# Performance work log

Measured on AMD Instinct MI355X. Metric: run time of the kernel, lower is better.

## Reference

```python
import jax, jax.numpy as jnp
import numpy as np

B, T, DIM = 2, 4096, 2048
H, HKV = 16, 4
HD = DIM // H          # 128
NREP = H // HKV        # 4
R = 16                 # csa_compress_ratio
TOPK = 64              # min(csa_top_k, max_seq_len // R)
THETA = 10000.0


def setup_inputs() -> dict:
    key = jax.random.key(0)
    ks = jax.random.split(key, 9)
    s = 0.02
    return {
        "x":   jax.random.normal(ks[0], (B, T, DIM), jnp.float32),
        "wq":  jax.random.normal(ks[1], (DIM, H * HD),  jnp.float32) * s,
        "wk":  jax.random.normal(ks[2], (DIM, HKV * HD), jnp.float32) * s,
        "wv":  jax.random.normal(ks[3], (DIM, HKV * HD), jnp.float32) * s,
        "wo":  jax.random.normal(ks[4], (DIM, DIM), jnp.float32) * s,
        "wiq": jax.random.normal(ks[5], (DIM, HD), jnp.float32) * s,
        "wik": jax.random.normal(ks[6], (DIM, HD), jnp.float32) * s,
        "cwa": jax.random.normal(ks[7], (HD,), jnp.float32) * s,
        "cwb": jax.random.normal(ks[8], (HD,), jnp.float32) * s,
    }


def _rope(x, cos, sin):
    # x: [B, h, T, HD]; pairs (x[2i], x[2i+1]) rotated by angle[t, i]
    half = HD // 2
    xr = x.reshape(*x.shape[:-1], half, 2)
    a, b = xr[..., 0], xr[..., 1]          # [B, h, T, half]
    ra = a * cos - b * sin                 # cos/sin: [T, half] broadcast
    rb = a * sin + b * cos
    return jnp.stack([ra, rb], axis=-1).reshape(x.shape)


def reference(x, wq, wk, wv, wo, wiq, wik, cwa, cwb):
    Bx, Tx, C = x.shape
    half = HD // 2
    # RoPE tables (buffer in original, deterministic -> recomputed here)
    freqs = 1.0 / (THETA ** (jnp.arange(half, dtype=jnp.float32) / half))
    ang = jnp.arange(Tx, dtype=jnp.float32)[:, None] * freqs[None, :]  # [T, half]
    cos, sin = jnp.cos(ang), jnp.sin(ang)

    q = (x @ wq).reshape(Bx, Tx, H, HD).transpose(0, 2, 1, 3)    # [B,H,T,HD]
    k = (x @ wk).reshape(Bx, Tx, HKV, HD).transpose(0, 2, 1, 3)  # [B,HKV,T,HD]
    v = (x @ wv).reshape(Bx, Tx, HKV, HD).transpose(0, 2, 1, 3)
    q = _rope(q, cos, sin)
    k = _rope(k, cos, sin)

    # chunked softmax-weighted KV compression (vectorized over blocks)
    nb = Tx // R
    kb = k.reshape(Bx, HKV, nb, R, HD)
    vb = v.reshape(Bx, HKV, nb, R, HD)
    wa = jax.nn.softmax(kb @ cwa, axis=-1)   # [B,HKV,nb,R], softmax within block
    wb_ = jax.nn.softmax(kb @ cwb, axis=-1)
    w = 0.5 * (wa + wb_)
    ck = jnp.einsum('bhnr,bhnrd->bhnd', w, kb)  # [B,HKV,nb,HD]
    cv = jnp.einsum('bhnr,bhnrd->bhnd', w, vb)

    # indexer: scores[b,t] = mean_j( qi[b,t] . ki[b,j] ) = qi[b,t] . mean_j ki[b,j]
    qi = x @ wiq                         # [B,T,HD]
    ki_mean = (x @ wik).mean(axis=1)     # [B,HD]
    scores = jnp.einsum('btd,bd->bt', qi, ki_mean)  # [B,T]
    block_scores = scores[:, :nb]                   # [B,nb]

    if nb > TOPK:
        idx = jax.lax.top_k(block_scores, TOPK)[1]             # [B,TOPK]
        ck = jnp.take_along_axis(ck, idx[:, None, :, None], axis=2)  # [B,HKV,TOPK,HD]
        cv = jnp.take_along_axis(cv, idx[:, None, :, None], axis=2)

    # GQA repeat + sparse attention over selected compressed blocks (no mask)
    k_rep = jnp.repeat(ck, NREP, axis=1)   # [B,H,TOPK,HD]
    v_rep = jnp.repeat(cv, NREP, axis=1)
    att = jax.nn.softmax(
        jnp.einsum('bhtd,bhsd->bhts', q, k_rep) / jnp.sqrt(jnp.float32(HD)),
        axis=-1)                            # [B,H,T,TOPK]
    out = jnp.einsum('bhts,bhsd->bhtd', att, v_rep)
    out = out.transpose(0, 2, 1, 3).reshape(Bx, Tx, C)
    return out @ wo
```

## Files before the change

kernel.cpp:

```cpp
#include <hip/hip_runtime.h>
#include <math.h>
#include <stdint.h>

#define BB    2
#define TT    4096
#define CDIM  2048
#define NHQ   16
#define NKV   4
#define HD    128
#define HALF  64
#define NREP  4
#define RBLK  16
#define NB    256
#define TOPK  64

#define MROWS (BB * TT)
#define NQKV  (CDIM + 2 * NKV * HD)
#define XELE  ((size_t)MROWS * CDIM)

typedef __bf16 bf16;
typedef __bf16 bf16x4 __attribute__((ext_vector_type(4)));
typedef __bf16 bf16x8 __attribute__((ext_vector_type(8)));
typedef float f32x4 __attribute__((ext_vector_type(4)));

typedef __attribute__((address_space(1))) unsigned int gu32;
typedef __attribute__((address_space(3))) unsigned int lu32;

__device__ __forceinline__ void gload_lds16(const void* g, void* l) {
  void* gv = const_cast<void*>(g);
  __builtin_amdgcn_global_load_lds((gu32*)gv, (lu32*)l, 16, 0, 0);
}

#define MFMA_BF16 __builtin_amdgcn_mfma_f32_16x16x32_bf16


#define LB192   28672
#define A192_AL 8192
#define A192_BH 16384
#define A192_BL 22528

__device__ __forceinline__ void mfma3_core192(const bf16* __restrict__ Ah,
                                              const bf16* __restrict__ Al,
                                              const bf16* __restrict__ Bh,
                                              const bf16* __restrict__ Bl,
                                              int bm, int bn,
                                              f32x4 acc[8][3]) {
  __shared__ __align__(16) bf16 smem[2 * LB192];
  const int tid = threadIdx.x;
  const int wave = tid >> 6, lane = tid & 63;
  const int lr4 = lane >> 2;
  const int cgs = (lane & 3) ^ ((lane >> 3) & 3);
  const size_t stageoff = (size_t)lr4 * CDIM + cgs * 8;

  const bf16* gp[7];
  int loff[7];
#pragma unroll
  for (int u = 0; u < 7; ++u) {
    int c = wave * 7 + u;
    const bf16* base;
    int lb;
    if (c < 16)      { base = Ah + (size_t)(bm + c * 16) * CDIM;        lb = c * 512; }
    else if (c < 32) { base = Al + (size_t)(bm + (c - 16) * 16) * CDIM; lb = A192_AL + (c - 16) * 512; }
    else if (c < 44) { base = Bh + (size_t)(bn + (c - 32) * 16) * CDIM; lb = A192_BH + (c - 32) * 512; }
    else             { base = Bl + (size_t)(bn + (c - 44) * 16) * CDIM; lb = A192_BL + (c - 44) * 512; }
    gp[u] = base + stageoff;
    loff[u] = lb;
  }

  const int wr = wave >> 2, wc = wave & 3;
  const int fr = lane & 15, lg = lane >> 4;
  const int chunk = (lg ^ ((fr >> 1) & 3)) << 3;
  const int arow = wr * 128 + fr;
  const int brow = wc * 48 + fr;

#pragma unroll
  for (int u = 0; u < 7; ++u) gload_lds16(gp[u], &smem[loff[u]]);

  for (int t = 0; t < 64; ++t) {
    const bf16* cb = &smem[(t & 1) * LB192];
    bf16* nb = &smem[((t + 1) & 1) * LB192];
    const int kk = (t + 1) * 32;
    const bool nlast = (t < 63);

    if (nlast) {
      gload_lds16(gp[0] + kk, nb + loff[0]);
      gload_lds16(gp[1] + kk, nb + loff[1]);
      gload_lds16(gp[2] + kk, nb + loff[2]);
      asm volatile("s_waitcnt vmcnt(3)" ::: "memory");
    } else {
      asm volatile("s_waitcnt vmcnt(0)" ::: "memory");
    }
    __builtin_amdgcn_s_barrier();
    asm volatile("" ::: "memory");

    bf16x8 fah[8], fal[8];
#pragma unroll
    for (int i = 0; i < 8; ++i) {
      fah[i] = *(const bf16x8*)&cb[(arow + i * 16) * 32 + chunk];
      fal[i] = *(const bf16x8*)&cb[A192_AL + (arow + i * 16) * 32 + chunk];
    }
    {
      bf16x8 fbh = *(const bf16x8*)&cb[A192_BH + brow * 32 + chunk];
      bf16x8 fbl = *(const bf16x8*)&cb[A192_BL + brow * 32 + chunk];
      __builtin_amdgcn_s_setprio(1);
#pragma unroll
      for (int i = 0; i < 8; ++i) {
        acc[i][0] = MFMA_BF16(fah[i], fbh, acc[i][0], 0, 0, 0);
        acc[i][0] = MFMA_BF16(fah[i], fbl, acc[i][0], 0, 0, 0);
        acc[i][0] = MFMA_BF16(fal[i], fbh, acc[i][0], 0, 0, 0);
      }
      __builtin_amdgcn_s_setprio(0);
    }
    asm volatile("" ::: "memory");
    __builtin_amdgcn_s_barrier();
    asm volatile("" ::: "memory");

#pragma unroll
    for (int j = 1; j < 3; ++j) {
      if (nlast) {
        gload_lds16(gp[2 * j + 1] + kk, nb + loff[2 * j + 1]);
        gload_lds16(gp[2 * j + 2] + kk, nb + loff[2 * j + 2]);
      }
      bf16x8 fbh = *(const bf16x8*)&cb[A192_BH + (brow + j * 16) * 32 + chunk];
      bf16x8 fbl = *(const bf16x8*)&cb[A192_BL + (brow + j * 16) * 32 + chunk];
      asm volatile("" ::: "memory");
      __builtin_amdgcn_s_barrier();
      __builtin_amdgcn_s_setprio(1);
#pragma unroll
      for (int i = 0; i < 8; ++i) {
        acc[i][j] = MFMA_BF16(fah[i], fbh, acc[i][j], 0, 0, 0);
        acc[i][j] = MFMA_BF16(fah[i], fbl, acc[i][j], 0, 0, 0);
        acc[i][j] = MFMA_BF16(fal[i], fbh, acc[i][j], 0, 0, 0);
      }
      __builtin_amdgcn_s_setprio(0);
      asm volatile("" ::: "memory");
      __builtin_amdgcn_s_barrier();
      asm volatile("" ::: "memory");
    }
  }
}

#define LDS_BUF 32768
#define OFF_AL  8192
#define OFF_BH  16384
#define OFF_BL  24576

__device__ __forceinline__ void mfma3_core256(const bf16* __restrict__ Ah,
                                              const bf16* __restrict__ Al,
                                              const bf16* __restrict__ Bh,
                                              const bf16* __restrict__ Bl,
                                              int bm, int bn,
                                              f32x4 acc[8][4]) {
  __shared__ __align__(16) bf16 smem[2 * LDS_BUF];
  const int tid = threadIdx.x;
  const int wave = tid >> 6, lane = tid & 63;
  const int lr4 = lane >> 2;
  const int cgs = (lane & 3) ^ ((lane >> 3) & 3);
  const size_t stageoff = (size_t)lr4 * CDIM + cgs * 8;

  const bf16* gp[8];
  int loff[8];
#pragma unroll
  for (int u = 0; u < 8; ++u) {
    int c = wave * 8 + u;
    const bf16* base;
    int lb;
    if (c < 16)      { base = Ah + (size_t)(bm + c * 16) * CDIM;        lb = c * 512; }
    else if (c < 32) { base = Al + (size_t)(bm + (c - 16) * 16) * CDIM; lb = OFF_AL + (c - 16) * 512; }
    else if (c < 48) { base = Bh + (size_t)(bn + (c - 32) * 16) * CDIM; lb = OFF_BH + (c - 32) * 512; }
    else             { base = Bl + (size_t)(bn + (c - 48) * 16) * CDIM; lb = OFF_BL + (c - 48) * 512; }
    gp[u] = base + stageoff;
    loff[u] = lb;
  }

  const int wr = wave >> 2, wc = wave & 3;
  const int fr = lane & 15, lg = lane >> 4;
  const int chunk = (lg ^ ((fr >> 1) & 3)) << 3;
  const int arow = wr * 128 + fr;
  const int brow = wc * 64 + fr;

#pragma unroll
  for (int u = 0; u < 8; ++u) gload_lds16(gp[u], &smem[loff[u]]);

  for (int t = 0; t < 64; ++t) {
    const bf16* cb = &smem[(t & 1) * LDS_BUF];
    bf16* nb = &smem[((t + 1) & 1) * LDS_BUF];
    const int kk = (t + 1) * 32;
    const bool nlast = (t < 63);

    if (nlast) {
      gload_lds16(gp[0] + kk, nb + loff[0]);
      gload_lds16(gp[1] + kk, nb + loff[1]);
      asm volatile("s_waitcnt vmcnt(2)" ::: "memory");
    } else {
      asm volatile("s_waitcnt vmcnt(0)" ::: "memory");
    }
    __builtin_amdgcn_s_barrier();
    asm volatile("" ::: "memory");

    bf16x8 fah[8], fal[8];
#pragma unroll
    for (int i = 0; i < 8; ++i) {
      fah[i] = *(const bf16x8*)&cb[(arow + i * 16) * 32 + chunk];
      fal[i] = *(const bf16x8*)&cb[OFF_AL + (arow + i * 16) * 32 + chunk];
    }
    {
      bf16x8 fbh = *(const bf16x8*)&cb[OFF_BH + brow * 32 + chunk];
      bf16x8 fbl = *(const bf16x8*)&cb[OFF_BL + brow * 32 + chunk];
      __builtin_amdgcn_s_setprio(1);
#pragma unroll
      for (int i = 0; i < 8; ++i) {
        acc[i][0] = MFMA_BF16(fah[i], fbh, acc[i][0], 0, 0, 0);
        acc[i][0] = MFMA_BF16(fah[i], fbl, acc[i][0], 0, 0, 0);
        acc[i][0] = MFMA_BF16(fal[i], fbh, acc[i][0], 0, 0, 0);
      }
      __builtin_amdgcn_s_setprio(0);
    }
    asm volatile("" ::: "memory");
    __builtin_amdgcn_s_barrier();
    asm volatile("" ::: "memory");

#pragma unroll
    for (int j = 1; j < 4; ++j) {
      if (nlast) {
        gload_lds16(gp[2 * j] + kk, nb + loff[2 * j]);
        gload_lds16(gp[2 * j + 1] + kk, nb + loff[2 * j + 1]);
      }
      bf16x8 fbh = *(const bf16x8*)&cb[OFF_BH + (brow + j * 16) * 32 + chunk];
      bf16x8 fbl = *(const bf16x8*)&cb[OFF_BL + (brow + j * 16) * 32 + chunk];
      asm volatile("" ::: "memory");
      __builtin_amdgcn_s_barrier();
      __builtin_amdgcn_s_setprio(1);
#pragma unroll
      for (int i = 0; i < 8; ++i) {
        acc[i][j] = MFMA_BF16(fah[i], fbh, acc[i][j], 0, 0, 0);
        acc[i][j] = MFMA_BF16(fah[i], fbl, acc[i][j], 0, 0, 0);
        acc[i][j] = MFMA_BF16(fal[i], fbh, acc[i][j], 0, 0, 0);
      }
      __builtin_amdgcn_s_setprio(0);
      asm volatile("" ::: "memory");
      __builtin_amdgcn_s_barrier();
      asm volatile("" ::: "memory");
    }
  }
}

__device__ __forceinline__ void xcd_swizzle(int& by, int& bx) {
  const int nwgx = gridDim.x;
  const int nwg = nwgx * gridDim.y;
  const int cpx = nwg >> 3;
  const int bid = blockIdx.y * nwgx + blockIdx.x;
  const int l = (bid & 7) * cpx + (bid >> 3);
  by = l / nwgx;
  bx = l - by * nwgx;
}

__global__ __launch_bounds__(512, 1) void csa_gemm_qkv(const bf16* __restrict__ xh,
                                                       const bf16* __restrict__ xl,
                                                       const bf16* __restrict__ wth,
                                                       const bf16* __restrict__ wtl,
                                                       float* __restrict__ qb,
                                                       float* __restrict__ kb,
                                                       float* __restrict__ vb) {
  f32x4 acc[8][3] = {};
  int by, bx;
  xcd_swizzle(by, bx);
  const int bm = by << 8, bn = bx * 192;
  mfma3_core192(xh, xl, wth, wtl, bm, bn, acc);
  const int wave = threadIdx.x >> 6, lane = threadIdx.x & 63;
  const int wr = wave >> 2, wc = wave & 3;
  const int fr = lane & 15, lg = lane >> 4;
#pragma unroll
  for (int j = 0; j < 3; ++j) {
    int cg = bn + wc * 48 + j * 16;
    float* dst; int ncols, c0;
    if (cg < CDIM)            { dst = qb; ncols = CDIM; c0 = cg; }
    else if (cg < CDIM + 512) { dst = kb; ncols = 512;  c0 = cg - CDIM; }
    else                      { dst = vb; ncols = 512;  c0 = cg - CDIM - 512; }
    int col = c0 + fr;
#pragma unroll
    for (int i = 0; i < 8; ++i) {
      int row0 = bm + wr * 128 + i * 16 + (lg << 2);
#pragma unroll
      for (int r = 0; r < 4; ++r)
        dst[(size_t)(row0 + r) * ncols + col] = acc[i][j][r];
    }
  }
}

__global__ __launch_bounds__(512, 1) void csa_gemm_wo(const bf16* __restrict__ ah,
                                                      const bf16* __restrict__ al,
                                                      const bf16* __restrict__ wth,
                                                      const bf16* __restrict__ wtl,
                                                      float* __restrict__ C) {
  f32x4 acc[8][4] = {};
  int by, bx;
  xcd_swizzle(by, bx);
  const int bm = by << 8, bn = bx << 8;
  mfma3_core256(ah, al, wth, wtl, bm, bn, acc);
  const int wave = threadIdx.x >> 6, lane = threadIdx.x & 63;
  const int wr = wave >> 2, wc = wave & 3;
  const int fr = lane & 15, lg = lane >> 4;
#pragma unroll
  for (int i = 0; i < 8; ++i)
#pragma unroll
    for (int j = 0; j < 4; ++j) {
      int row0 = bm + wr * 128 + i * 16 + (lg << 2);
      int col = bn + wc * 64 + j * 16 + fr;
#pragma unroll
      for (int r = 0; r < 4; ++r)
        C[(size_t)(row0 + r) * CDIM + col] = acc[i][j][r];
    }
}

__global__ void csa_xconv(const float4* __restrict__ x, bf16x4* __restrict__ xh,
                          bf16x4* __restrict__ xl) {
  int i = blockIdx.x * 256 + threadIdx.x;
  float4 v = x[i];
  bf16x4 h, l;
  h[0] = (bf16)v.x; l[0] = (bf16)(v.x - (float)h[0]);
  h[1] = (bf16)v.y; l[1] = (bf16)(v.y - (float)h[1]);
  h[2] = (bf16)v.z; l[2] = (bf16)(v.z - (float)h[2]);
  h[3] = (bf16)v.w; l[3] = (bf16)(v.w - (float)h[3]);
  xh[i] = h;
  xl[i] = l;
}

__global__ __launch_bounds__(256) void csa_wconv(const float* __restrict__ W, int N,
                                                 bf16* __restrict__ wth,
                                                 bf16* __restrict__ wtl, int rowofs) {
  __shared__ float tile[32][33];
  int k0 = blockIdx.y * 32, n0 = blockIdx.x * 32;
  int tx = threadIdx.x & 31, ty = threadIdx.x >> 5;
#pragma unroll
  for (int r = 0; r < 32; r += 8)
    tile[ty + r][tx] = W[(size_t)(k0 + ty + r) * N + n0 + tx];
  __syncthreads();
#pragma unroll
  for (int r = 0; r < 32; r += 8) {
    int n = ty + r;
    float x = tile[tx][n];
    bf16 h = (bf16)x;
    bf16 l = (bf16)(x - (float)h);
    size_t o = (size_t)(rowofs + n0 + n) * CDIM + k0 + tx;
    wth[o] = h;
    wtl[o] = l;
  }
}

__global__ void csa_rope_table(float* __restrict__ cost, float* __restrict__ sint) {
  int idx = blockIdx.x * blockDim.x + threadIdx.x;
  if (idx >= TT * HALF) return;
  int t = idx / HALF, i = idx % HALF;
  double freq = pow(10000.0, -(double)i / (double)HALF);
  double ang = (double)t * freq;
  cost[idx] = (float)cos(ang);
  sint[idx] = (float)sin(ang);
}

__global__ void csa_rope_apply(float* __restrict__ buf, const float* __restrict__ cost,
                               const float* __restrict__ sint, int nheads, int total) {
  int idx = blockIdx.x * blockDim.x + threadIdx.x;
  if (idx >= total) return;
  int i = idx % HALF;
  int h = (idx / HALF) % nheads;
  int t = (idx / (HALF * nheads)) % TT;
  int b = idx / (HALF * nheads * TT);
  float c = cost[t * HALF + i], s = sint[t * HALF + i];
  float* p = buf + ((((size_t)b * TT + t) * nheads + h) * HD) + 2 * i;
  float a = p[0], q = p[1];
  p[0] = a * c - q * s;
  p[1] = a * s + q * c;
}

__global__ void csa_xpart(const float* __restrict__ x, float* __restrict__ xpart) {
  int d = blockIdx.x * 256 + threadIdx.x;
  int ts = blockIdx.y;
  int b = blockIdx.z;
  float s = 0.f;
  int t0 = ts * (TT / 16);
  for (int t = t0; t < t0 + TT / 16; ++t) s += x[((size_t)b * TT + t) * CDIM + d];
  xpart[((size_t)b * 16 + ts) * CDIM + d] = s;
}

__global__ void csa_kimean(const float* __restrict__ xpart, const float* __restrict__ wik,
                           float* __restrict__ ki) {
  int b = blockIdx.x >> 7;
  int j = blockIdx.x & 127;
  int tid = threadIdx.x;
  float s = 0.f;
  for (int d = tid; d < CDIM; d += 256) {
    float xm = 0.f;
#pragma unroll
    for (int ts = 0; ts < 16; ++ts) xm += xpart[((size_t)b * 16 + ts) * CDIM + d];
    s += xm * wik[(size_t)d * HD + j];
  }
  __shared__ float red[256];
  red[tid] = s;
  __syncthreads();
  for (int off = 128; off > 0; off >>= 1) {
    if (tid < off) red[tid] += red[tid + off];
    __syncthreads();
  }
  if (tid == 0) ki[b * HD + j] = red[0] * (1.f / (float)TT);
}

__global__ void csa_u(const float* __restrict__ wiq, const float* __restrict__ ki,
                      float* __restrict__ u) {
  int idx = blockIdx.x * 256 + threadIdx.x;
  int b = idx / CDIM, d = idx % CDIM;
  float s = 0.f;
#pragma unroll 8
  for (int j = 0; j < HD; ++j) s += wiq[(size_t)d * HD + j] * ki[b * HD + j];
  u[idx] = s;
}

__global__ void csa_scores(const float* __restrict__ x, const float* __restrict__ u,
                           float* __restrict__ sc) {
  int b = blockIdx.x >> 8;
  int t = blockIdx.x & 255;
  int tid = threadIdx.x;
  float s = 0.f;
  for (int d = tid; d < CDIM; d += 256)
    s += x[((size_t)b * TT + t) * CDIM + d] * u[b * CDIM + d];
  __shared__ float red[256];
  red[tid] = s;
  __syncthreads();
  for (int off = 128; off > 0; off >>= 1) {
    if (tid < off) red[tid] += red[tid + off];
    __syncthreads();
  }
  if (tid == 0) sc[blockIdx.x] = red[0];
}

__global__ void csa_topk(const float* __restrict__ sc, int* __restrict__ topk) {
  __shared__ float val[NB];
  __shared__ float rv[256];
  __shared__ int ri[256];
  int b = blockIdx.x, tid = threadIdx.x;
  val[tid] = sc[b * NB + tid];
  __syncthreads();
  for (int it = 0; it < TOPK; ++it) {
    rv[tid] = val[tid];
    ri[tid] = tid;
    __syncthreads();
    for (int off = 128; off > 0; off >>= 1) {
      if (tid < off) {
        if (rv[tid + off] > rv[tid] ||
            (rv[tid + off] == rv[tid] && ri[tid + off] < ri[tid])) {
          rv[tid] = rv[tid + off];
          ri[tid] = ri[tid + off];
        }
      }
      __syncthreads();
    }
    if (tid == 0) {
      topk[b * TOPK + it] = ri[0];
      val[ri[0]] = -INFINITY;
    }
    __syncthreads();
  }
}

__global__ __launch_bounds__(64) void csa_compress(const float* __restrict__ kbuf,
                                                   const float* __restrict__ vbuf,
                                                   const int* __restrict__ topk,
                                                   const float* __restrict__ cwa,
                                                   const float* __restrict__ cwb,
                                                   bf16* __restrict__ ckh,
                                                   bf16* __restrict__ ckl,
                                                   bf16* __restrict__ cvth,
                                                   bf16* __restrict__ cvtl) {
  int blk = blockIdx.x;
  int b = blk / (NKV * TOPK);
  int h = (blk / TOPK) % NKV;
  int j = blk % TOPK;
  int n = topk[b * TOPK + j];
  int l = threadIdx.x;
  float ca0 = cwa[l], ca1 = cwa[l + 64];
  float cb0 = cwb[l], cb1 = cwb[l + 64];
  float kk[RBLK][2], vv[RBLK][2], ar[RBLK], br[RBLK];
#pragma unroll
  for (int r = 0; r < RBLK; ++r) {
    int t = n * RBLK + r;
    size_t base = (((size_t)b * TT + t) * NKV + h) * HD;
    kk[r][0] = kbuf[base + l];
    kk[r][1] = kbuf[base + l + 64];
    vv[r][0] = vbuf[base + l];
    vv[r][1] = vbuf[base + l + 64];
    float pa = kk[r][0] * ca0 + kk[r][1] * ca1;
    float pb = kk[r][0] * cb0 + kk[r][1] * cb1;
    for (int off = 32; off > 0; off >>= 1) {
      pa += __shfl_xor(pa, off);
      pb += __shfl_xor(pb, off);
    }
    ar[r] = pa;
    br[r] = pb;
  }
  float ma = -INFINITY, mb = -INFINITY;
#pragma unroll
  for (int r = 0; r < RBLK; ++r) { ma = fmaxf(ma, ar[r]); mb = fmaxf(mb, br[r]); }
  float ea[RBLK], eb[RBLK], sa = 0.f, sb = 0.f;
#pragma unroll
  for (int r = 0; r < RBLK; ++r) {
    ea[r] = expf(ar[r] - ma); sa += ea[r];
    eb[r] = expf(br[r] - mb); sb += eb[r];
  }
  float isa = 1.f / sa, isb = 1.f / sb;
  float o0 = 0.f, o1 = 0.f, p0 = 0.f, p1 = 0.f;
#pragma unroll
  for (int r = 0; r < RBLK; ++r) {
    float w = 0.5f * (ea[r] * isa + eb[r] * isb);
    o0 += w * kk[r][0]; o1 += w * kk[r][1];
    p0 += w * vv[r][0]; p1 += w * vv[r][1];
  }
  size_t ckbase = ((size_t)(b * NKV + h) * 64 + j) * 128;
  bf16 h0 = (bf16)o0; ckh[ckbase + l] = h0;      ckl[ckbase + l] = (bf16)(o0 - (float)h0);
  bf16 h1 = (bf16)o1; ckh[ckbase + l + 64] = h1; ckl[ckbase + l + 64] = (bf16)(o1 - (float)h1);
  size_t vtbase = (size_t)(b * NKV + h) * (128 * 64);
  bf16 g0 = (bf16)p0; cvth[vtbase + (size_t)l * 64 + j] = g0;
  cvtl[vtbase + (size_t)l * 64 + j] = (bf16)(p0 - (float)g0);
  bf16 g1 = (bf16)p1; cvth[vtbase + (size_t)(l + 64) * 64 + j] = g1;
  cvtl[vtbase + (size_t)(l + 64) * 64 + j] = (bf16)(p1 - (float)g1);
}

__global__ __launch_bounds__(256) void csa_attn_mfma(const float* __restrict__ qb,
                                                     const float* __restrict__ cost,
                                                     const float* __restrict__ sint,
                                                     const bf16* __restrict__ ckh_g,
                                                     const bf16* __restrict__ ckl_g,
                                                     const bf16* __restrict__ cvth_g,
                                                     const bf16* __restrict__ cvtl_g,
                                                     bf16* __restrict__ oh_g,
                                                     bf16* __restrict__ ol_g) {
  __shared__ __align__(16) bf16 sck[2][64 * 128];
  __shared__ __align__(16) bf16 sV[2][64 * 64];
  const int tid = threadIdx.x;
  const int wave = tid >> 6, lane = tid & 63;
  const int b = blockIdx.y >> 2, kvh = blockIdx.y & 3;
  const int row0 = blockIdx.x << 7;
  const int wrow = wave << 5;
  const int lr = lane & 15, lg = lane >> 4;
  const float scale = 0.08838834764831845f;

  const bf16* gkh = ckh_g + (size_t)(b * NKV + kvh) * (64 * 128);
  const bf16* gkl = ckl_g + (size_t)(b * NKV + kvh) * (64 * 128);
  const bf16* gvh = cvth_g + (size_t)(b * NKV + kvh) * (128 * 64);
  const bf16* gvl = cvtl_g + (size_t)(b * NKV + kvh) * (128 * 64);

  for (int idx = tid; idx < 1024; idx += 256) {
    int j = idx >> 4, c = idx & 15;
    int dst = (j * 16 + (c ^ (j & 15))) * 8;
    *(uint4*)&sck[0][dst] = *(const uint4*)(gkh + j * 128 + c * 8);
    *(uint4*)&sck[1][dst] = *(const uint4*)(gkl + j * 128 + c * 8);
  }
  for (int idx = tid; idx < 512; idx += 256) {
    int d = idx >> 3, c = idx & 7;
    int dst = (d * 8 + (c ^ (d & 7))) * 8;
    *(uint4*)&sV[0][dst] = *(const uint4*)(gvh + d * 64 + c * 8);
    *(uint4*)&sV[1][dst] = *(const uint4*)(gvl + d * 64 + c * 8);
  }

  bf16x8 qfh[2][4], qfl[2][4];
#pragma unroll
  for (int it = 0; it < 2; ++it)
#pragma unroll
    for (int ks = 0; ks < 4; ++ks) {
      int row = wrow + it * 16 + lr;
      int g = row0 + row;
      int t = g >> 2;
      int hh = kvh * NREP + (g & 3);
      int d0 = ks * 32 + (lg << 3);
      const float* qp = qb + (((size_t)b * TT + t) * NHQ + hh) * HD + d0;
      float4 a = *(const float4*)qp;
      float4 b4 = *(const float4*)(qp + 4);
      float4 cs = *(const float4*)&cost[t * HALF + (d0 >> 1)];
      float4 sn = *(const float4*)&sint[t * HALF + (d0 >> 1)];
      float f[8];
      f[0] = a.x * cs.x - a.y * sn.x;  f[1] = a.x * sn.x + a.y * cs.x;
      f[2] = a.z * cs.y - a.w * sn.y;  f[3] = a.z * sn.y + a.w * cs.y;
      f[4] = b4.x * cs.z - b4.y * sn.z; f[5] = b4.x * sn.z + b4.y * cs.z;
      f[6] = b4.z * cs.w - b4.w * sn.w; f[7] = b4.z * sn.w + b4.w * cs.w;
      bf16x8 h8, l8;
#pragma unroll
      for (int u = 0; u < 8; ++u) {
        h8[u] = (bf16)f[u];
        l8[u] = (bf16)(f[u] - (float)h8[u]);
      }
      qfh[it][ks] = h8;
      qfl[it][ks] = l8;
    }
  __syncthreads();

  f32x4 accS[2][4] = {};
#pragma unroll
  for (int ks = 0; ks < 4; ++ks) {
    bf16x8 kh[4], kl[4];
#pragma unroll
    for (int jt = 0; jt < 4; ++jt) {
      int row = jt * 16 + lr;
      int c = ks * 4 + lg;
      int off = (row * 16 + (c ^ (row & 15))) * 8;
      kh[jt] = *(const bf16x8*)&sck[0][off];
      kl[jt] = *(const bf16x8*)&sck[1][off];
    }
#pragma unroll
    for (int it = 0; it < 2; ++it)
#pragma unroll
      for (int jt = 0; jt < 4; ++jt) {
        accS[it][jt] = MFMA_BF16(qfh[it][ks], kh[jt], accS[it][jt], 0, 0, 0);
        accS[it][jt] = MFMA_BF16(qfh[it][ks], kl[jt], accS[it][jt], 0, 0, 0);
        accS[it][jt] = MFMA_BF16(qfl[it][ks], kh[jt], accS[it][jt], 0, 0, 0);
      }
  }

#pragma unroll
  for (int it = 0; it < 2; ++it)
#pragma unroll
    for (int r = 0; r < 4; ++r) {
      float v0 = accS[it][0][r] * scale, v1 = accS[it][1][r] * scale;
      float v2 = accS[it][2][r] * scale, v3 = accS[it][3][r] * scale;
      float m = fmaxf(fmaxf(v0, v1), fmaxf(v2, v3));
      for (int off = 8; off > 0; off >>= 1) m = fmaxf(m, __shfl_xor(m, off));
      float e0 = expf(v0 - m), e1 = expf(v1 - m), e2 = expf(v2 - m), e3 = expf(v3 - m);
      float s = e0 + e1 + e2 + e3;
      for (int off = 8; off > 0; off >>= 1) s += __shfl_xor(s, off);
      float inv = 1.f / s;
      accS[it][0][r] = e0 * inv; accS[it][1][r] = e1 * inv;
      accS[it][2][r] = e2 * inv; accS[it][3][r] = e3 * inv;
    }

  __syncthreads();

#pragma unroll
  for (int it = 0; it < 2; ++it)
#pragma unroll
    for (int jt = 0; jt < 4; ++jt)
#pragma unroll
      for (int r = 0; r < 4; ++r) {
        int row = wrow + it * 16 + (lg << 2) + r;
        int k = jt * 16 + lr;
        float p = accS[it][jt][r];
        bf16 ph = (bf16)p;
        int c = k >> 3;
        int off = (row * 8 + (c ^ (row & 7))) * 8 + (k & 7);
        sck[0][off] = ph;
        sck[1][off] = (bf16)(p - (float)ph);
      }
  __syncthreads();

  for (int half = 0; half < 2; ++half) {
    if (half) {
      __syncthreads();
      for (int idx = tid; idx < 512; idx += 256) {
        int d = idx >> 3, c = idx & 7;
        int dst = (d * 8 + (c ^ (d & 7))) * 8;
        *(uint4*)&sV[0][dst] = *(const uint4*)(gvh + (64 + d) * 64 + c * 8);
        *(uint4*)&sV[1][dst] = *(const uint4*)(gvl + (64 + d) * 64 + c * 8);
      }
      __syncthreads();
    }
    f32x4 accO[2][4] = {};
#pragma unroll
    for (int ks = 0; ks < 2; ++ks) {
      bf16x8 pah[2], pal[2], vh[4], vl[4];
#pragma unroll
      for (int it = 0; it < 2; ++it) {
        int row = wrow + it * 16 + lr;
        int c = ks * 4 + lg;
        int off = (row * 8 + (c ^ (row & 7))) * 8;
        pah[it] = *(const bf16x8*)&sck[0][off];
        pal[it] = *(const bf16x8*)&sck[1][off];
      }
#pragma unroll
      for (int jt = 0; jt < 4; ++jt) {
        int d = jt * 16 + lr;
        int c = ks * 4 + lg;
        int off = (d * 8 + (c ^ (d & 7))) * 8;
        vh[jt] = *(const bf16x8*)&sV[0][off];
        vl[jt] = *(const bf16x8*)&sV[1][off];
      }
#pragma unroll
      for (int it = 0; it < 2; ++it)
#pragma unroll
        for (int jt = 0; jt < 4; ++jt) {
          accO[it][jt] = MFMA_BF16(pah[it], vh[jt], accO[it][jt], 0, 0, 0);
          accO[it][jt] = MFMA_BF16(pah[it], vl[jt], accO[it][jt], 0, 0, 0);
          accO[it][jt] = MFMA_BF16(pal[it], vh[jt], accO[it][jt], 0, 0, 0);
        }
    }
#pragma unroll
    for (int it = 0; it < 2; ++it)
#pragma unroll
      for (int jt = 0; jt < 4; ++jt)
#pragma unroll
        for (int r = 0; r < 4; ++r) {
          int row = wrow + it * 16 + (lg << 2) + r;
          int g = row0 + row;
          int t = g >> 2;
          int hh = kvh * NREP + (g & 3);
          size_t ob = (((size_t)b * TT + t) * NHQ + hh) * HD + half * 64 + jt * 16 + lr;
          float o = accO[it][jt][r];
          bf16 oh = (bf16)o;
          oh_g[ob] = oh;
          ol_g[ob] = (bf16)(o - (float)oh);
        }
  }
}

extern "C" void kernel_launch(void* const* d_in, const int* in_sizes, int n_in,
                              void* d_out, int out_size, void* d_ws, size_t ws_size,
                              hipStream_t stream) {
  const float* x   = (const float*)d_in[0];
  const float* wq  = (const float*)d_in[1];
  const float* wk  = (const float*)d_in[2];
  const float* wv  = (const float*)d_in[3];
  const float* wo  = (const float*)d_in[4];
  const float* wiq = (const float*)d_in[5];
  const float* wik = (const float*)d_in[6];
  const float* cwa = (const float*)d_in[7];
  const float* cwb = (const float*)d_in[8];
  float* out = (float*)d_out;

  float* qb = out;

  float* ws = (float*)d_ws;
  float* kb   = ws;
  float* vb   = kb + (size_t)MROWS * 512;
  bf16*  xh   = (bf16*)(vb + (size_t)MROWS * 512);
  bf16*  xl   = xh + XELE;
  bf16*  wqh  = xl + XELE;
  bf16*  wql  = wqh + (size_t)NQKV * CDIM;
  float* cost = (float*)(wql + (size_t)NQKV * CDIM);
  float* sint = cost + (size_t)TT * HALF;
  float* xpart = sint + (size_t)TT * HALF;
  float* ki   = xpart + (size_t)BB * 16 * CDIM;
  float* u    = ki + BB * HD;
  float* sc   = u + BB * CDIM;
  bf16*  ckh  = (bf16*)(sc + BB * NB);
  bf16*  ckl  = ckh + (size_t)BB * NKV * 64 * 128;
  bf16*  cvth = ckl + (size_t)BB * NKV * 64 * 128;
  bf16*  cvtl = cvth + (size_t)BB * NKV * 128 * 64;
  int* topk   = (int*)(cvtl + (size_t)BB * NKV * 128 * 64);
  bf16* oh  = xh;
  bf16* ol_ = xl;
  bf16* woh = wqh;
  bf16* wol = wql;

  csa_xconv<<<(XELE / 4) / 256, 256, 0, stream>>>((const float4*)x, (bf16x4*)xh, (bf16x4*)xl);
  csa_wconv<<<dim3(CDIM / 32, CDIM / 32), 256, 0, stream>>>(wq, CDIM, wqh, wql, 0);
  csa_wconv<<<dim3(512 / 32, CDIM / 32), 256, 0, stream>>>(wk, 512, wqh, wql, CDIM);
  csa_wconv<<<dim3(512 / 32, CDIM / 32), 256, 0, stream>>>(wv, 512, wqh, wql, CDIM + 512);

  csa_gemm_qkv<<<dim3(NQKV / 192, MROWS / 256), 512, 0, stream>>>(xh, xl, wqh, wql, qb, kb, vb);

  csa_wconv<<<dim3(CDIM / 32, CDIM / 32), 256, 0, stream>>>(wo, CDIM, woh, wol, 0);

  csa_rope_table<<<(TT * HALF + 255) / 256, 256, 0, stream>>>(cost, sint);
  csa_rope_apply<<<(BB * TT * NKV * HALF + 255) / 256, 256, 0, stream>>>(kb, cost, sint, NKV, BB * TT * NKV * HALF);

  csa_xpart<<<dim3(CDIM / 256, 16, BB), 256, 0, stream>>>(x, xpart);
  csa_kimean<<<BB * HD, 256, 0, stream>>>(xpart, wik, ki);
  csa_u<<<(BB * CDIM) / 256, 256, 0, stream>>>(wiq, ki, u);
  csa_scores<<<BB * NB, 256, 0, stream>>>(x, u, sc);
  csa_topk<<<BB, 256, 0, stream>>>(sc, topk);

  csa_compress<<<BB * NKV * TOPK, 64, 0, stream>>>(kb, vb, topk, cwa, cwb, ckh, ckl, cvth, cvtl);

  csa_attn_mfma<<<dim3((TT * NREP) / 128, BB * NKV), 256, 0, stream>>>(qb, cost, sint, ckh, ckl, cvth, cvtl, oh, ol_);

  csa_gemm_wo<<<dim3(CDIM / 256, MROWS / 256), 512, 0, stream>>>(oh, ol_, woh, wol, out);
}
```

Before: 735.3 us.

## Merge weight conversions, use bitonic sort for top-k, add MFMA priority hints

Merges the three wq/wk/wv transpose-and-split conversion launches into one kernel that picks its source matrix from the block index, removing two launches. Replaces the 64-round iterative argmax top-k with a single bitonic sort of the 256 scores, keeping the same tie-breaking order. Wraps the MFMA loops in the attention kernel with s_setprio raises to favour waves in their matrix phase. These are small, separate tweaks to minor kernels and scheduling, with little change to the dominant GEMM cost.

Result: faster. 657.6 us (median of 2 runs) (-10.6%).

```diff
diff --git a/kernel.cpp b/kernel.cpp
--- a/kernel.cpp
+++ b/kernel.cpp
@@ -348,6 +348,35 @@
   }
 }
 
+__global__ __launch_bounds__(256) void csa_wconv3(const float* __restrict__ wq,
+                                                  const float* __restrict__ wk,
+                                                  const float* __restrict__ wv,
+                                                  bf16* __restrict__ wth,
+                                                  bf16* __restrict__ wtl) {
+  __shared__ float tile[32][33];
+  int bx = blockIdx.x;
+  const float* W; int N, rowofs, n0;
+  if (bx < 64)      { W = wq; N = 2048; rowofs = 0;    n0 = bx * 32; }
+  else if (bx < 80) { W = wk; N = 512;  rowofs = 2048; n0 = (bx - 64) * 32; }
+  else              { W = wv; N = 512;  rowofs = 2560; n0 = (bx - 80) * 32; }
+  int k0 = blockIdx.y * 32;
+  int tx = threadIdx.x & 31, ty = threadIdx.x >> 5;
+#pragma unroll
+  for (int r = 0; r < 32; r += 8)
+    tile[ty + r][tx] = W[(size_t)(k0 + ty + r) * N + n0 + tx];
+  __syncthreads();
+#pragma unroll
+  for (int r = 0; r < 32; r += 8) {
+    int n = ty + r;
+    float x = tile[tx][n];
+    bf16 h = (bf16)x;
+    bf16 l = (bf16)(x - (float)h);
+    size_t o = (size_t)(rowofs + n0 + n) * CDIM + k0 + tx;
+    wth[o] = h;
+    wtl[o] = l;
+  }
+}
+
 __global__ void csa_rope_table(float* __restrict__ cost, float* __restrict__ sint) {
   int idx = blockIdx.x * blockDim.x + threadIdx.x;
   if (idx >= TT * HALF) return;
@@ -433,33 +462,31 @@
   if (tid == 0) sc[blockIdx.x] = red[0];
 }
 
-__global__ void csa_topk(const float* __restrict__ sc, int* __restrict__ topk) {
-  __shared__ float val[NB];
-  __shared__ float rv[256];
-  __shared__ int ri[256];
+__global__ __launch_bounds__(256) void csa_topk(const float* __restrict__ sc,
+                                                int* __restrict__ topk) {
+  __shared__ float v[NB];
+  __shared__ int ix[NB];
   int b = blockIdx.x, tid = threadIdx.x;
-  val[tid] = sc[b * NB + tid];
+  v[tid] = sc[b * NB + tid];
+  ix[tid] = tid;
   __syncthreads();
-  for (int it = 0; it < TOPK; ++it) {
-    rv[tid] = val[tid];
-    ri[tid] = tid;
-    __syncthreads();
-    for (int off = 128; off > 0; off >>= 1) {
-      if (tid < off) {
-        if (rv[tid + off] > rv[tid] ||
-            (rv[tid + off] == rv[tid] && ri[tid + off] < ri[tid])) {
-          rv[tid] = rv[tid + off];
-          ri[tid] = ri[tid + off];
+  for (int k = 2; k <= NB; k <<= 1) {
+    for (int j = k >> 1; j > 0; j >>= 1) {
+      int p = tid ^ j;
+      if (p > tid) {
+        float va = v[tid], vb = v[p];
+        int ia = ix[tid], ib = ix[p];
+        bool abefore = (va > vb) || (va == vb && ia < ib);
+        bool up = ((tid & k) == 0);
+        if (up ? !abefore : abefore) {
+          v[tid] = vb; ix[tid] = ib;
+          v[p] = va;  ix[p] = ia;
         }
       }
       __syncthreads();
     }
-    if (tid == 0) {
-      topk[b * TOPK + it] = ri[0];
-      val[ri[0]] = -INFINITY;
-    }
-    __syncthreads();
-  }
+  }
+  if (tid < TOPK) topk[b * TOPK + tid] = ix[tid];
 }
 
 __global__ __launch_bounds__(64) void csa_compress(const float* __restrict__ kbuf,
@@ -604,6 +631,7 @@
       kh[jt] = *(const bf16x8*)&sck[0][off];
       kl[jt] = *(const bf16x8*)&sck[1][off];
     }
+    __builtin_amdgcn_s_setprio(1);
 #pragma unroll
     for (int it = 0; it < 2; ++it)
 #pragma unroll
@@ -612,6 +640,7 @@
         accS[it][jt] = MFMA_BF16(qfh[it][ks], kl[jt], accS[it][jt], 0, 0, 0);
         accS[it][jt] = MFMA_BF16(qfl[it][ks], kh[jt], accS[it][jt], 0, 0, 0);
       }
+    __builtin_amdgcn_s_setprio(0);
   }
 
 #pragma unroll
@@ -680,6 +709,7 @@
         vh[jt] = *(const bf16x8*)&sV[0][off];
         vl[jt] = *(const bf16x8*)&sV[1][off];
       }
+      __builtin_amdgcn_s_setprio(1);
 #pragma unroll
       for (int it = 0; it < 2; ++it)
 #pragma unroll
@@ -688,6 +718,7 @@
           accO[it][jt] = MFMA_BF16(pah[it], vl[jt], accO[it][jt], 0, 0, 0);
           accO[it][jt] = MFMA_BF16(pal[it], vh[jt], accO[it][jt], 0, 0, 0);
         }
+      __builtin_amdgcn_s_setprio(0);
     }
 #pragma unroll
     for (int it = 0; it < 2; ++it)
@@ -748,9 +779,7 @@
   bf16* wol = wql;
 
   csa_xconv<<<(XELE / 4) / 256, 256, 0, stream>>>((const float4*)x, (bf16x4*)xh, (bf16x4*)xl);
-  csa_wconv<<<dim3(CDIM / 32, CDIM / 32), 256, 0, stream>>>(wq, CDIM, wqh, wql, 0);
-  csa_wconv<<<dim3(512 / 32, CDIM / 32), 256, 0, stream>>>(wk, 512, wqh, wql, CDIM);
-  csa_wconv<<<dim3(512 / 32, CDIM / 32), 256, 0, stream>>>(wv, 512, wqh, wql, CDIM + 512);
+  csa_wconv3<<<dim3(96, CDIM / 32), 256, 0, stream>>>(wq, wk, wv, wqh, wql);
 
   csa_gemm_qkv<<<dim3(NQKV / 192, MROWS / 256), 512, 0, stream>>>(xh, xl, wqh, wql, qb, kb, vb);
 
```
